# Kernel tuning notes

Hardware: AMD Instinct MI355X
Metric: run time of the kernel (lower is better)

The kernel has to match this reference:

```python
import jax, jax.numpy as jnp
import numpy as np
import math

HIDDEN = 512
NUM_HEADS = 8
HEAD_DIM = HIDDEN // NUM_HEADS
NUM_BUCKETS = 32
MAX_DISTANCE = 128


def _relative_position_bucket(rel_pos, bidirectional=True):
    # rel_pos: int32 [S, T]
    num_buckets = NUM_BUCKETS
    ret = 0
    if bidirectional:
        num_buckets //= 2
        ret = (rel_pos > 0).astype(jnp.int32) * num_buckets
        rel_pos = jnp.abs(rel_pos)
    else:
        rel_pos = -jnp.minimum(rel_pos, 0)
    max_exact = num_buckets // 2
    is_small = rel_pos < max_exact
    # guard log(0); result unused where is_small
    safe = jnp.maximum(rel_pos, 1).astype(jnp.float32)
    val_if_large = max_exact + (
        jnp.log(safe / max_exact) / math.log(MAX_DISTANCE / max_exact) * (num_buckets - max_exact)
    ).astype(jnp.int32)
    val_if_large = jnp.minimum(val_if_large, num_buckets - 1)
    return ret + jnp.where(is_small, rel_pos, val_if_large)


def setup_inputs() -> dict:
    key = jax.random.key(0)
    ks = jax.random.split(key, 6)
    B, S = 4, 2048
    std = 1.0 / math.sqrt(HIDDEN)
    inp = {
        "x": jax.random.normal(ks[0], (B, S, HIDDEN), dtype=jnp.float32),
        "Wq": jax.random.normal(ks[1], (HIDDEN, HIDDEN), dtype=jnp.float32) * std,
        "Wk": jax.random.normal(ks[2], (HIDDEN, HIDDEN), dtype=jnp.float32) * std,
        "Wv": jax.random.normal(ks[3], (HIDDEN, HIDDEN), dtype=jnp.float32) * std,
        "Wo": jax.random.normal(ks[4], (HIDDEN, HIDDEN), dtype=jnp.float32) * std,
        "bias_table": jax.random.normal(ks[5], (NUM_BUCKETS, NUM_HEADS), dtype=jnp.float32) * 0.02,
    }
    return inp


def reference(x, Wq, Wk, Wv, Wo, bias_table):
    # x: [B, S, HIDDEN]; weights: [HIDDEN, HIDDEN] (out = x @ W.T semantics folded as x @ W here
    # -- weights are random so orientation is a convention; we use x @ W).
    B, S, _ = x.shape
    T = S  # self-attention, context=None
    scale = HEAD_DIM ** -0.5

    def split_heads(t, L):
        return t.reshape(B, L, NUM_HEADS, HEAD_DIM).transpose(0, 2, 1, 3)  # [B,H,L,D]

    q = split_heads(x @ Wq, S)
    k = split_heads(x @ Wk, T)
    v = split_heads(x @ Wv, T)

    # relative position bias: [1, H, S, T]
    rel = jnp.arange(T, dtype=jnp.int32)[None, :] - jnp.arange(S, dtype=jnp.int32)[:, None]
    buckets = _relative_position_bucket(rel, bidirectional=True)  # [S, T]
    pos_bias = bias_table[buckets]  # [S, T, H]
    pos_bias = pos_bias.transpose(2, 0, 1)[None]  # [1, H, S, T]

    attn = jnp.einsum("bhsd,bhtd->bhst", q, k) * scale + pos_bias
    attn = jax.nn.softmax(attn, axis=-1)  # dropout = identity (eval)
    out = jnp.einsum("bhst,bhtd->bhsd", attn, v)
    out = out.transpose(0, 2, 1, 3).reshape(B, S, HIDDEN)
    return out @ Wo
```

## Files before the change

### kernel.cpp

```cpp
#include <hip/hip_runtime.h>
#include <hip/hip_bf16.h>
#include <math.h>

#define HIDDEN 512
#define NHEADS 8
#define HDIM 64
#define SLEN 2048
#define BATCH 4
#define NROWS (BATCH*SLEN)
#define RTAB (2*SLEN-1)
#define LOG2E 1.44269504088896340736f
#define SCALE_L2E (0.125f * LOG2E)

typedef _Float16 f16;
typedef f16 f16x8 __attribute__((ext_vector_type(8)));
typedef float f32x4 __attribute__((ext_vector_type(4)));
typedef unsigned short u16;
typedef unsigned int u32;
typedef u16 u16x8 __attribute__((ext_vector_type(8)));
typedef u32 u32x4 __attribute__((ext_vector_type(4)));

__global__ __launch_bounds__(256) void bias_precompute(
    const float* __restrict__ bias_table, float* __restrict__ biasrel) {
  int i = blockIdx.x * 256 + threadIdx.x;
  if (i >= NHEADS * RTAB) return;
  int h = i / RTAB;
  int idx = i - h * RTAB;
  int rel = idx - (SLEN - 1);
  int ret = rel > 0 ? 16 : 0;
  int a = rel < 0 ? -rel : rel;
  int bidx;
  if (a < 8) {
    bidx = a;
  } else {
    float val = logf((float)a * 0.125f) / logf(16.0f) * 8.0f;
    bidx = 8 + (int)val;
    if (bidx > 15) bidx = 15;
  }
  biasrel[i] = bias_table[(ret + bidx) * NHEADS + h] * LOG2E;
}

__global__ __launch_bounds__(256) void conv_x(
    const float* __restrict__ x, u16* __restrict__ xh) {
  int i = blockIdx.x * 256 + threadIdx.x;
  const float4* p = (const float4*)(x + (size_t)i * 8);
  float4 a = p[0], b = p[1];
  u16x8 o;
  f16 t0 = (f16)a.x; o[0] = *(u16*)&t0;
  f16 t1 = (f16)a.y; o[1] = *(u16*)&t1;
  f16 t2 = (f16)a.z; o[2] = *(u16*)&t2;
  f16 t3 = (f16)a.w; o[3] = *(u16*)&t3;
  f16 t4 = (f16)b.x; o[4] = *(u16*)&t4;
  f16 t5 = (f16)b.y; o[5] = *(u16*)&t5;
  f16 t6 = (f16)b.z; o[6] = *(u16*)&t6;
  f16 t7 = (f16)b.w; o[7] = *(u16*)&t7;
  *(u16x8*)(xh + (size_t)i * 8) = o;
}

__global__ __launch_bounds__(256) void conv_w(
    const float* __restrict__ Wq, const float* __restrict__ Wk,
    const float* __restrict__ Wv, const float* __restrict__ Wo,
    u16* __restrict__ Wt) {
  const float* W = blockIdx.y == 0 ? Wq : blockIdx.y == 1 ? Wk
                 : blockIdx.y == 2 ? Wv : Wo;
  u16* dst = Wt + (size_t)blockIdx.y * HIDDEN * HIDDEN;
  int t = blockIdx.x * 256 + threadIdx.x;
  int k = t >> 6, n0 = (t & 63) << 3;
  const float4* p = (const float4*)(W + (size_t)k * HIDDEN + n0);
  float4 a = p[0], b = p[1];
  float vals[8] = {a.x, a.y, a.z, a.w, b.x, b.y, b.z, b.w};
#pragma unroll
  for (int j = 0; j < 8; ++j) {
    f16 hv = (f16)vals[j];
    dst[(size_t)(n0 + j) * HIDDEN + k] = *(u16*)&hv;
  }
}

__global__ __launch_bounds__(256) void gemm_mfma(
    const u16* __restrict__ A, const u16* __restrict__ Wt0,
    const u16* __restrict__ Wt1, const u16* __restrict__ Wt2,
    void* __restrict__ O, int mode) {
  __shared__ u16 As[128][72];
  __shared__ u16 Bs[128][72];
  const u16* Wt = blockIdx.z == 0 ? Wt0 : blockIdx.z == 1 ? Wt1 : Wt2;
  const int tid = threadIdx.x;
  const int w = tid >> 6, l = tid & 63;
  const int lr = l & 15, lg = l >> 4;
  const int wr = w >> 1, wc = w & 1;
  const int m0 = blockIdx.x << 7, n0 = blockIdx.y << 7;
  const int vtmode = (mode == 1) && (blockIdx.z == 2);

  f32x4 acc[4][4] = {};

  for (int k0 = 0; k0 < HIDDEN; k0 += 64) {
    __syncthreads();
#pragma unroll
    for (int e = 0; e < 4; ++e) {
      int c = (e << 8) + tid;
      int row = c >> 3, g = c & 7;
      *(u16x8*)&As[row][g << 3] =
          *(const u16x8*)(A + (size_t)(m0 + row) * HIDDEN + k0 + (g << 3));
      *(u16x8*)&Bs[row][g << 3] =
          *(const u16x8*)(Wt + (size_t)(n0 + row) * HIDDEN + k0 + (g << 3));
    }
    __syncthreads();
#pragma unroll
    for (int kk = 0; kk < 64; kk += 32) {
      f16x8 af[4], bf[4];
#pragma unroll
      for (int mt = 0; mt < 4; ++mt)
        af[mt] = *(const f16x8*)&As[(wr << 6) + (mt << 4) + lr][kk + (lg << 3)];
#pragma unroll
      for (int nt = 0; nt < 4; ++nt)
        bf[nt] = *(const f16x8*)&Bs[(wc << 6) + (nt << 4) + lr][kk + (lg << 3)];
      if (!vtmode) {
#pragma unroll
        for (int mt = 0; mt < 4; ++mt)
#pragma unroll
          for (int nt = 0; nt < 4; ++nt)
            acc[mt][nt] = __builtin_amdgcn_mfma_f32_16x16x32_f16(
                af[mt], bf[nt], acc[mt][nt], 0, 0, 0);
      } else {
#pragma unroll
        for (int i = 0; i < 4; ++i)
#pragma unroll
          for (int j = 0; j < 4; ++j)
            acc[i][j] = __builtin_amdgcn_mfma_f32_16x16x32_f16(
                bf[i], af[j], acc[i][j], 0, 0, 0);
      }
    }
  }

  if (mode == 0) {
    float* Of = (float*)O;
#pragma unroll
    for (int mt = 0; mt < 4; ++mt)
#pragma unroll
      for (int nt = 0; nt < 4; ++nt)
#pragma unroll
        for (int r = 0; r < 4; ++r) {
          int m = m0 + (wr << 6) + (mt << 4) + (lg << 2) + r;
          int n = n0 + (wc << 6) + (nt << 4) + lr;
          Of[(size_t)m * HIDDEN + n] = acc[mt][nt][r];
        }
  } else if (!vtmode) {
    u16* O16 = (u16*)O + (size_t)blockIdx.z * NROWS * HIDDEN;
    const float osc = (blockIdx.z == 0) ? SCALE_L2E : 1.0f;
#pragma unroll
    for (int mt = 0; mt < 4; ++mt)
#pragma unroll
      for (int nt = 0; nt < 4; ++nt)
#pragma unroll
        for (int r = 0; r < 4; ++r) {
          int m = m0 + (wr << 6) + (mt << 4) + (lg << 2) + r;
          int n = n0 + (wc << 6) + (nt << 4) + lr;
          int b = m >> 11, s = m & (SLEN - 1);
          int h = n >> 6, d = n & 63;
          f16 hv = (f16)(acc[mt][nt][r] * osc);
          O16[(((size_t)b * NHEADS + h) * SLEN + s) * HDIM + d] = *(u16*)&hv;
        }
  } else {
    u16* O16 = (u16*)O + (size_t)2 * NROWS * HIDDEN;
#pragma unroll
    for (int i = 0; i < 4; ++i)
#pragma unroll
      for (int j = 0; j < 4; ++j)
#pragma unroll
        for (int r = 0; r < 4; ++r) {
          int n = n0 + (wc << 6) + (i << 4) + (lg << 2) + r;
          int m = m0 + (wr << 6) + (j << 4) + lr;
          int b = m >> 11, s = m & (SLEN - 1);
          int h = n >> 6, d = n & 63;
          int u = s & 31;
          int p = (((u & 15) >> 2) << 3) + (u & 3) + ((u >> 4) << 2);
          int ss = (s & ~31) | p;
          f16 hv = (f16)acc[i][j][r];
          O16[(((size_t)b * NHEADS + h) * HDIM + d) * SLEN + ss] = *(u16*)&hv;
        }
  }
}

__global__ __launch_bounds__(256) void flash_attn_mfma(
    const u16* __restrict__ qg, const u16* __restrict__ kg,
    const u16* __restrict__ vtg, const float* __restrict__ biasrel,
    u16* __restrict__ attn_out) {
  __shared__ u16 Ks[64][72];
  __shared__ u16 Vt[64][72];

  const int tid = threadIdx.x;
  const int w = tid >> 6, l = tid & 63;
  const int lr = l & 15, lg = l >> 4;

  int bid = blockIdx.x;
  int xcd = bid & 7, idx = bid >> 3;
  int bh = (xcd << 2) + (idx >> 4);
  int bx = idx & 15;
  int h = bh & 7, b = bh >> 3;
  int q0 = bx << 7;

  const u16* qp = qg + (size_t)bh * (SLEN * HDIM);
  const u16* kp = kg + (size_t)bh * (SLEN * HDIM);
  const u16* vp = vtg + (size_t)bh * (HDIM * SLEN);

  const float bias_pos = biasrel[h * RTAB + 2 * (SLEN - 1)];
  const float bias_neg = biasrel[h * RTAB];

  f16x8 aq[2][2];
#pragma unroll
  for (int sub = 0; sub < 2; ++sub) {
    const u16* qrow = qp + (size_t)(q0 + (w << 5) + (sub << 4) + lr) * HDIM + (lg << 3);
    aq[sub][0] = *(const f16x8*)(qrow);
    aq[sub][1] = *(const f16x8*)(qrow + 32);
  }

  const float* bb = biasrel + h * RTAB + (SLEN - 1) + (lg << 2) - lr - q0 - (w << 5);

  f32x4 acc[2][4] = {};
  float l_run[2] = {0.f, 0.f};

  u16x8 kreg[2], vreg[2];
#pragma unroll
  for (int e = 0; e < 2; ++e) {
    int c = tid + (e << 8);
    int row = c >> 3, c8 = (c & 7) << 3;
    kreg[e] = *(const u16x8*)(kp + (size_t)row * HDIM + c8);
    vreg[e] = *(const u16x8*)(vp + (size_t)row * SLEN + c8);
  }

  for (int t0 = 0; t0 < SLEN; t0 += 64) {
    __syncthreads();
#pragma unroll
    for (int e = 0; e < 2; ++e) {
      int c = tid + (e << 8);
      int row = c >> 3, c8 = (c & 7) << 3;
      *(u16x8*)&Ks[row][c8] = kreg[e];
      *(u16x8*)&Vt[row][c8] = vreg[e];
    }
    __syncthreads();

    if (t0 + 64 < SLEN) {
#pragma unroll
      for (int e = 0; e < 2; ++e) {
        int c = tid + (e << 8);
        int row = c >> 3, c8 = (c & 7) << 3;
        kreg[e] = *(const u16x8*)(kp + (size_t)(t0 + 64 + row) * HDIM + c8);
        vreg[e] = *(const u16x8*)(vp + (size_t)row * SLEN + t0 + 64 + c8);
      }
    }

    int dtq = t0 - q0;
    f32x4 sc[2][4];
    if (dtq >= 256 || dtq <= -192) {
      float c = (dtq > 0) ? bias_pos : bias_neg;
      f32x4 cv = {c, c, c, c};
#pragma unroll
      for (int sub = 0; sub < 2; ++sub)
#pragma unroll
        for (int ct = 0; ct < 4; ++ct) sc[sub][ct] = cv;
    } else {
#pragma unroll
      for (int sub = 0; sub < 2; ++sub)
#pragma unroll
        for (int ct = 0; ct < 4; ++ct)
#pragma unroll
          for (int r = 0; r < 4; ++r)
            sc[sub][ct][r] = bb[t0 + (ct << 4) + r - (sub << 4)];
    }

    f16x8 kf[4][2];
#pragma unroll
    for (int ct = 0; ct < 4; ++ct) {
      kf[ct][0] = *(const f16x8*)&Ks[(ct << 4) + lr][lg << 3];
      kf[ct][1] = *(const f16x8*)&Ks[(ct << 4) + lr][32 + (lg << 3)];
    }

    __builtin_amdgcn_s_setprio(1);
#pragma unroll
    for (int sub = 0; sub < 2; ++sub)
#pragma unroll
      for (int ct = 0; ct < 4; ++ct) {
        sc[sub][ct] = __builtin_amdgcn_mfma_f32_16x16x32_f16(
            kf[ct][0], aq[sub][0], sc[sub][ct], 0, 0, 0);
        sc[sub][ct] = __builtin_amdgcn_mfma_f32_16x16x32_f16(
            kf[ct][1], aq[sub][1], sc[sub][ct], 0, 0, 0);
      }
    __builtin_amdgcn_s_setprio(0);

#pragma unroll
    for (int sub = 0; sub < 2; ++sub) {
      float rs = 0.f;
#pragma unroll
      for (int ct = 0; ct < 4; ++ct)
#pragma unroll
        for (int r = 0; r < 4; ++r) {
          float pe = __builtin_amdgcn_exp2f(sc[sub][ct][r]);
          sc[sub][ct][r] = pe;
          rs += pe;
        }
      l_run[sub] += rs;
    }

    f16x8 vf[2][4];
#pragma unroll
    for (int kb = 0; kb < 2; ++kb)
#pragma unroll
      for (int dt = 0; dt < 4; ++dt)
        vf[kb][dt] = *(const f16x8*)&Vt[(dt << 4) + lr][(kb << 5) + (lg << 3)];

    __builtin_amdgcn_s_setprio(1);
#pragma unroll
    for (int sub = 0; sub < 2; ++sub)
#pragma unroll
      for (int kb = 0; kb < 2; ++kb) {
        u32 a0 = __builtin_bit_cast(u32,
            __builtin_amdgcn_cvt_pkrtz(sc[sub][2 * kb][0], sc[sub][2 * kb][1]));
        u32 a1 = __builtin_bit_cast(u32,
            __builtin_amdgcn_cvt_pkrtz(sc[sub][2 * kb][2], sc[sub][2 * kb][3]));
        u32 a2 = __builtin_bit_cast(u32,
            __builtin_amdgcn_cvt_pkrtz(sc[sub][2 * kb + 1][0], sc[sub][2 * kb + 1][1]));
        u32 a3 = __builtin_bit_cast(u32,
            __builtin_amdgcn_cvt_pkrtz(sc[sub][2 * kb + 1][2], sc[sub][2 * kb + 1][3]));
        u32x4 pk = {a0, a1, a2, a3};
        f16x8 pa = __builtin_bit_cast(f16x8, pk);
#pragma unroll
        for (int dt = 0; dt < 4; ++dt)
          acc[sub][dt] = __builtin_amdgcn_mfma_f32_16x16x32_f16(
              pa, vf[kb][dt], acc[sub][dt], 0, 0, 0);
      }
    __builtin_amdgcn_s_setprio(0);
  }

#pragma unroll
  for (int sub = 0; sub < 2; ++sub) {
    float lt = l_run[sub];
    lt += __shfl_xor(lt, 16, 64);
    lt += __shfl_xor(lt, 32, 64);
    float linv[4];
#pragma unroll
    for (int r = 0; r < 4; ++r) linv[r] = 1.f / __shfl(lt, (lg << 2) + r, 16);
    u16* op = attn_out +
              ((size_t)(b * SLEN) + q0 + (w << 5) + (sub << 4)) * HIDDEN + (h << 6);
#pragma unroll
    for (int r = 0; r < 4; ++r)
#pragma unroll
      for (int dt = 0; dt < 4; ++dt) {
        f16 hv = (f16)(acc[sub][dt][r] * linv[r]);
        op[(size_t)((lg << 2) + r) * HIDDEN + (dt << 4) + lr] = *(u16*)&hv;
      }
  }
}

extern "C" void kernel_launch(void* const* d_in, const int* in_sizes, int n_in,
                              void* d_out, int out_size, void* d_ws, size_t ws_size,
                              hipStream_t stream) {
  const float* x          = (const float*)d_in[0];
  const float* Wq         = (const float*)d_in[1];
  const float* Wk         = (const float*)d_in[2];
  const float* Wv         = (const float*)d_in[3];
  const float* Wo         = (const float*)d_in[4];
  const float* bias_table = (const float*)d_in[5];
  float* out = (float*)d_out;

  u16* xh   = (u16*)d_ws;
  u16* wt   = xh + (size_t)NROWS * HIDDEN;
  u16* qkv  = wt + (size_t)4 * HIDDEN * HIDDEN;
  u16* attno_h = qkv + (size_t)3 * NROWS * HIDDEN;
  float* biasrel = (float*)(attno_h + (size_t)NROWS * HIDDEN);

  u16* qb = qkv;
  u16* kb = qkv + (size_t)NROWS * HIDDEN;
  u16* vb = qkv + (size_t)2 * NROWS * HIDDEN;

  bias_precompute<<<(NHEADS * RTAB + 255) / 256, 256, 0, stream>>>(bias_table, biasrel);
  conv_x<<<NROWS * HIDDEN / 8 / 256, 256, 0, stream>>>(x, xh);
  conv_w<<<dim3(HIDDEN * HIDDEN / 8 / 256, 4), 256, 0, stream>>>(Wq, Wk, Wv, Wo, wt);

  u16* wtq = wt;
  u16* wtk = wt + (size_t)HIDDEN * HIDDEN;
  u16* wtv = wt + (size_t)2 * HIDDEN * HIDDEN;
  u16* wto = wt + (size_t)3 * HIDDEN * HIDDEN;

  gemm_mfma<<<dim3(NROWS / 128, HIDDEN / 128, 3), 256, 0, stream>>>(
      xh, wtq, wtk, wtv, qkv, 1);

  flash_attn_mfma<<<SLEN / 128 * BATCH * NHEADS, 256, 0, stream>>>(
      qb, kb, vb, biasrel, attno_h);

  gemm_mfma<<<dim3(NROWS / 128, HIDDEN / 128, 1), 256, 0, stream>>>(
      attno_h, wto, wto, wto, out, 0);
}
```

Measured before the change: 108.6 us.

## Prefetch GEMM tiles into registers and stage V-transpose stores via LDS

The GEMM main loop now loads the next K-tile from global memory into registers while the current tile is being computed from shared memory, overlapping load latency with MFMA work. The V-transpose epilogue no longer issues scattered 2-byte global stores. It writes the accumulator tile into shared memory, then emits coalesced 16-byte stores that keep the permuted sequence order. This costs extra registers for the prefetch buffers and one extra LDS round-trip in the epilogue.

```diff
diff --git a/kernel.cpp b/kernel.cpp
--- a/kernel.cpp
+++ b/kernel.cpp
@@ -17,6 +17,7 @@
 typedef float f32x4 __attribute__((ext_vector_type(4)));
 typedef unsigned short u16;
 typedef unsigned int u32;
+typedef u16 u16x4 __attribute__((ext_vector_type(4)));
 typedef u16 u16x8 __attribute__((ext_vector_type(8)));
 typedef u32 u32x4 __attribute__((ext_vector_type(4)));
 
@@ -80,8 +81,9 @@
     const u16* __restrict__ A, const u16* __restrict__ Wt0,
     const u16* __restrict__ Wt1, const u16* __restrict__ Wt2,
     void* __restrict__ O, int mode) {
-  __shared__ u16 As[128][72];
-  __shared__ u16 Bs[128][72];
+  __shared__ u16 sm[2 * 128 * 72];
+  u16 (*As)[72] = (u16(*)[72])sm;
+  u16 (*Bs)[72] = (u16(*)[72])(sm + 128 * 72);
   const u16* Wt = blockIdx.z == 0 ? Wt0 : blockIdx.z == 1 ? Wt1 : Wt2;
   const int tid = threadIdx.x;
   const int w = tid >> 6, l = tid & 63;
@@ -92,18 +94,34 @@
 
   f32x4 acc[4][4] = {};
 
+  u16x8 areg[4], breg[4];
+#pragma unroll
+  for (int e = 0; e < 4; ++e) {
+    int c = (e << 8) + tid;
+    int row = c >> 3, g = c & 7;
+    areg[e] = *(const u16x8*)(A + (size_t)(m0 + row) * HIDDEN + (g << 3));
+    breg[e] = *(const u16x8*)(Wt + (size_t)(n0 + row) * HIDDEN + (g << 3));
+  }
+
   for (int k0 = 0; k0 < HIDDEN; k0 += 64) {
     __syncthreads();
 #pragma unroll
     for (int e = 0; e < 4; ++e) {
       int c = (e << 8) + tid;
       int row = c >> 3, g = c & 7;
-      *(u16x8*)&As[row][g << 3] =
-          *(const u16x8*)(A + (size_t)(m0 + row) * HIDDEN + k0 + (g << 3));
-      *(u16x8*)&Bs[row][g << 3] =
-          *(const u16x8*)(Wt + (size_t)(n0 + row) * HIDDEN + k0 + (g << 3));
-    }
-    __syncthreads();
+      *(u16x8*)&As[row][g << 3] = areg[e];
+      *(u16x8*)&Bs[row][g << 3] = breg[e];
+    }
+    __syncthreads();
+    if (k0 + 64 < HIDDEN) {
+#pragma unroll
+      for (int e = 0; e < 4; ++e) {
+        int c = (e << 8) + tid;
+        int row = c >> 3, g = c & 7;
+        areg[e] = *(const u16x8*)(A + (size_t)(m0 + row) * HIDDEN + k0 + 64 + (g << 3));
+        breg[e] = *(const u16x8*)(Wt + (size_t)(n0 + row) * HIDDEN + k0 + 64 + (g << 3));
+      }
+    }
 #pragma unroll
     for (int kk = 0; kk < 64; kk += 32) {
       f16x8 af[4], bf[4];
@@ -160,23 +178,38 @@
           O16[(((size_t)b * NHEADS + h) * SLEN + s) * HDIM + d] = *(u16*)&hv;
         }
   } else {
+    __syncthreads();
+    u16* tt = sm;
+#pragma unroll
+    for (int i = 0; i < 4; ++i)
+#pragma unroll
+      for (int j = 0; j < 4; ++j)
+#pragma unroll
+        for (int r = 0; r < 4; ++r) {
+          int nl = (wc << 6) + (i << 4) + (lg << 2) + r;
+          int ml = (wr << 6) + (j << 4) + lr;
+          f16 hv = (f16)acc[i][j][r];
+          tt[nl * 136 + ml] = *(u16*)&hv;
+        }
+    __syncthreads();
     u16* O16 = (u16*)O + (size_t)2 * NROWS * HIDDEN;
-#pragma unroll
-    for (int i = 0; i < 4; ++i)
-#pragma unroll
-      for (int j = 0; j < 4; ++j)
-#pragma unroll
-        for (int r = 0; r < 4; ++r) {
-          int n = n0 + (wc << 6) + (i << 4) + (lg << 2) + r;
-          int m = m0 + (wr << 6) + (j << 4) + lr;
-          int b = m >> 11, s = m & (SLEN - 1);
-          int h = n >> 6, d = n & 63;
-          int u = s & 31;
-          int p = (((u & 15) >> 2) << 3) + (u & 3) + ((u >> 4) << 2);
-          int ss = (s & ~31) | p;
-          f16 hv = (f16)acc[i][j][r];
-          O16[(((size_t)b * NHEADS + h) * HDIM + d) * SLEN + ss] = *(u16*)&hv;
-        }
+    int nl = tid >> 1, half = tid & 1;
+    int n = n0 + nl;
+    int h = n >> 6, d = n & 63;
+    int b = m0 >> 11, s_base = m0 & (SLEN - 1);
+    u16* orow = O16 + (((size_t)b * NHEADS + h) * HDIM + d) * SLEN + s_base;
+    const u16* trow = tt + nl * 136;
+#pragma unroll
+    for (int c = 0; c < 8; ++c) {
+      int v_off = (half << 6) + (c << 3);
+      int c0 = (v_off & ~31) | (((v_off >> 3) & 3) << 2);
+      u16x4 lo = *(const u16x4*)(trow + c0);
+      u16x4 hi = *(const u16x4*)(trow + c0 + 16);
+      u16x8 st;
+#pragma unroll
+      for (int j = 0; j < 4; ++j) { st[j] = lo[j]; st[j + 4] = hi[j]; }
+      *(u16x8*)(orow + v_off) = st;
+    }
   }
 }
 
```

After: 105.3 us. -3.0%, faster.
